# Performance work log

Measured on AMD Instinct MI355X. Metric: run time of the kernel, lower is better.

The kernel has to match this reference:

```python
import jax, jax.numpy as jnp
import numpy as np

B, N, F, H = 2, 2048, 1024, 16
HD = F // H
SQRT_D = float(np.sqrt(F))  # note: module scales by sqrt(in_c), not sqrt(head_dim)


def setup_inputs() -> dict:
    key = jax.random.key(0)
    ks = jax.random.split(key, 9)
    s = 1.0 / np.sqrt(F)
    mk = lambda k: jax.random.uniform(k, (F, F), jnp.float32, -s, s)
    mb = lambda k: jax.random.uniform(k, (F,), jnp.float32, -s, s)
    return {
        "x": jax.random.normal(ks[0], (B, N, F), jnp.float32),
        "Wq": mk(ks[1]), "bq": mb(ks[2]),
        "Wk": mk(ks[3]), "bk": mb(ks[4]),
        "Wv": mk(ks[5]), "bv": mb(ks[6]),
        "Wo": mk(ks[7]), "bo": mb(ks[8]),
    }


def reference(x, Wq, bq, Wk, bk, Wv, bv, Wo, bo):
    b, n, f = x.shape
    # projections (torch Linear: x @ W.T + b); view to (b, n, h, hd)
    q = (x @ Wq.T + bq).reshape(b, n, H, HD)
    k = (x @ Wk.T + bk).reshape(b, n, H, HD)
    v = (x @ Wv.T + bv).reshape(b, n, H, HD)
    score = jnp.einsum('bihd,bjhd->bhij', q, k)
    attn = jax.nn.softmax(score / SQRT_D, axis=-1)
    o = jnp.einsum('bhij,bjhd->bihd', attn, v).reshape(b, n, f)
    return o @ Wo.T + bo
```

## Files before the change

kernel.cpp:

```cpp
#include <hip/hip_runtime.h>
#include <hip/hip_bf16.h>
#include <stdint.h>
#include <stddef.h>

typedef __bf16 bf16;
typedef __attribute__((ext_vector_type(8))) __bf16 bf16x8;
typedef __attribute__((ext_vector_type(4))) __bf16 bf16x4;
typedef __attribute__((ext_vector_type(2))) __bf16 bf16x2;
typedef __attribute__((ext_vector_type(4))) float f32x4;

#define MFMA16(a, b, c) __builtin_amdgcn_mfma_f32_16x16x32_bf16(a, b, c, 0, 0, 0)

#define BB 2
#define SEQ 2048
#define FDIM 1024
#define NH 16
#define HD 64
#define M_TOK 4096
#define N_QKV 3072

#define CSC 0.04508422f

__device__ __forceinline__ void gll16(const bf16* g, bf16* l) {
    __builtin_amdgcn_global_load_lds(
        (const __attribute__((address_space(1))) void*)g,
        (__attribute__((address_space(3))) void*)l, 16, 0, 0);
}

__device__ __forceinline__ bf16 pack_bf16(float f) {
    uint32_t u = __builtin_bit_cast(uint32_t, f);
    uint16_t h = (uint16_t)((u + 0x8000u) >> 16);
    return __builtin_bit_cast(bf16, h);
}

__device__ __forceinline__ uint32_t pk2(float a, float b) {
#if __has_builtin(__builtin_amdgcn_cvt_pk_bf16_f32)
    bf16x2 t = __builtin_amdgcn_cvt_pk_bf16_f32(a, b);
    return __builtin_bit_cast(uint32_t, t);
#else
    uint32_t ua = __builtin_bit_cast(uint32_t, a) + 0x8000u;
    uint32_t ub = __builtin_bit_cast(uint32_t, b) + 0x8000u;
    return __builtin_amdgcn_perm(ub, ua, 0x07060302);
#endif
}

__global__ __launch_bounds__(256) void convert_k(
    const float* __restrict__ x,
    const float* __restrict__ Wq, const float* __restrict__ bq,
    const float* __restrict__ Wk, const float* __restrict__ bk,
    const float* __restrict__ Wv, const float* __restrict__ bv,
    const float* __restrict__ Wo,
    bf16* __restrict__ xb, bf16* __restrict__ Wcat, bf16* __restrict__ Wob,
    float* __restrict__ bcat)
{
    const int tid = blockIdx.x * blockDim.x + threadIdx.x;
    const int nt = gridDim.x * blockDim.x;
    const int NX4 = M_TOK * FDIM / 4;
    const int NW4 = FDIM * FDIM / 4;

    for (int i = tid; i < NX4; i += nt) {
        float4 v = ((const float4*)x)[i];
        bf16x4 o; o[0] = (bf16)v.x; o[1] = (bf16)v.y; o[2] = (bf16)v.z; o[3] = (bf16)v.w;
        ((bf16x4*)xb)[i] = o;
    }
    for (int i = tid; i < NW4; i += nt) {
        float4 v = ((const float4*)Wq)[i];
        bf16x4 o;
        o[0] = (bf16)(v.x * CSC); o[1] = (bf16)(v.y * CSC);
        o[2] = (bf16)(v.z * CSC); o[3] = (bf16)(v.w * CSC);
        ((bf16x4*)Wcat)[i] = o;
        v = ((const float4*)Wk)[i];
        o[0] = (bf16)v.x; o[1] = (bf16)v.y; o[2] = (bf16)v.z; o[3] = (bf16)v.w;
        ((bf16x4*)Wcat)[NW4 + i] = o;
        v = ((const float4*)Wv)[i];
        o[0] = (bf16)v.x; o[1] = (bf16)v.y; o[2] = (bf16)v.z; o[3] = (bf16)v.w;
        ((bf16x4*)Wcat)[2 * NW4 + i] = o;
        v = ((const float4*)Wo)[i];
        o[0] = (bf16)v.x; o[1] = (bf16)v.y; o[2] = (bf16)v.z; o[3] = (bf16)v.w;
        ((bf16x4*)Wob)[i] = o;
    }
    for (int i = tid; i < FDIM; i += nt) {
        bcat[i] = bq[i] * CSC;
        bcat[FDIM + i] = bk[i];
        bcat[2 * FDIM + i] = bv[i];
    }
}

__global__ __launch_bounds__(512, 2) void gemm256(
    const bf16* __restrict__ A,
    const bf16* __restrict__ Bw,
    const float* __restrict__ bias,
    bf16* __restrict__ Cb,
    bf16* __restrict__ VtOut,
    int M, int N, int K)
{
    extern __shared__ char smem[];
    const int tid = threadIdx.x;
    const int lane = tid & 63;
    const int wave = tid >> 6;
    const int wr = wave >> 2;
    const int wc = wave & 3;
    const int m0 = blockIdx.y * 256;
    const int n0 = blockIdx.x * 256;
    const int lrow = lane & 15;
    const int quad = lane >> 4;
    const int NT = K >> 6;

    const int l8 = lane >> 3;
    const int kx = ((lane & 7) ^ l8) << 3;
    const int lcl = wave * 16 + l8;

#define ASTG(sl, kt, mh, c) do { \
    const int _lc = lcl + (c) * 8; \
    const int _gr = m0 + ((_lc >> 6) << 7) + ((mh) << 6) + (_lc & 63); \
    gll16(A + (size_t)_gr * K + (size_t)(kt) * 64 + kx, \
          (bf16*)(smem + (sl) * 65536 + (mh) * 16384 + wave * 2048 + (c) * 1024)); \
} while (0)
#define BSTG(sl, kt, nh, c) do { \
    const int _lc = lcl + (c) * 8; \
    const int _gc = n0 + ((_lc >> 5) << 6) + ((nh) << 5) + (_lc & 31); \
    gll16(Bw + (size_t)_gc * K + (size_t)(kt) * 64 + kx, \
          (bf16*)(smem + (sl) * 65536 + 32768 + (nh) * 16384 + wave * 2048 + (c) * 1024)); \
} while (0)

    const int swz0 = ((quad ^ (lrow & 7)) << 4);
    const int swz1 = (((4 + quad) ^ (lrow & 7)) << 4);
    const int arow = (wr * 64 + lrow) * 128;
    const int brow = (wc * 32 + lrow) * 128;

    f32x4 acc[8][4] = {};
    bf16x8 af[4][2];
    bf16x8 bc[2][2][2];

    ASTG(0, 0, 0, 0); ASTG(0, 0, 0, 1);
    BSTG(0, 0, 0, 0); BSTG(0, 0, 0, 1);
    BSTG(0, 0, 1, 0); BSTG(0, 0, 1, 1);
    ASTG(0, 0, 1, 0); ASTG(0, 0, 1, 1);
    asm volatile("s_waitcnt vmcnt(4)" ::: "memory");
    __builtin_amdgcn_s_barrier();

    for (int t = 0; t < NT; ++t) {
        const int sl = t & 1;
        const int ns = sl ^ 1;
        const char* sb = smem + sl * 65536;
        const bool pf = (t + 1 < NT);

#pragma unroll
        for (int ph = 0; ph < 4; ++ph) {
            const int mh = ph >> 1, nh = ph & 1;
            if (pf) {
                if (ph == 0)      { ASTG(ns, t + 1, 0, 0); ASTG(ns, t + 1, 0, 1); }
                else if (ph == 1) { BSTG(ns, t + 1, 0, 0); BSTG(ns, t + 1, 0, 1); }
                else if (ph == 2) { BSTG(ns, t + 1, 1, 0); BSTG(ns, t + 1, 1, 1); }
                else              { ASTG(ns, t + 1, 1, 0); ASTG(ns, t + 1, 1, 1); }
            }
            if (nh == 0) {
#pragma unroll
                for (int iq = 0; iq < 4; ++iq) {
                    af[iq][0] = *(const bf16x8*)(sb + mh * 16384 + arow + iq * 2048 + swz0);
                    af[iq][1] = *(const bf16x8*)(sb + mh * 16384 + arow + iq * 2048 + swz1);
                }
            }
            if (ph == 0 || ph == 1) {
#pragma unroll
                for (int jq = 0; jq < 2; ++jq) {
                    bc[nh][jq][0] = *(const bf16x8*)(sb + 32768 + nh * 16384 + brow + jq * 2048 + swz0);
                    bc[nh][jq][1] = *(const bf16x8*)(sb + 32768 + nh * 16384 + brow + jq * 2048 + swz1);
                }
            }
            __builtin_amdgcn_s_setprio(1);
#pragma unroll
            for (int iq = 0; iq < 4; ++iq)
#pragma unroll
                for (int jq = 0; jq < 2; ++jq) {
                    acc[mh * 4 + iq][nh * 2 + jq] =
                        MFMA16(af[iq][0], bc[nh][jq][0], acc[mh * 4 + iq][nh * 2 + jq]);
                    acc[mh * 4 + iq][nh * 2 + jq] =
                        MFMA16(af[iq][1], bc[nh][jq][1], acc[mh * 4 + iq][nh * 2 + jq]);
                }
            __builtin_amdgcn_s_setprio(0);
            if (pf) asm volatile("s_waitcnt vmcnt(4)" ::: "memory");
            else    asm volatile("s_waitcnt vmcnt(0)" ::: "memory");
            __builtin_amdgcn_s_barrier();
        }
    }
#undef ASTG
#undef BSTG

    if (VtOut && n0 >= 2048) {
        const int bql = (m0 >> 11);
#pragma unroll
        for (int i = 0; i < 8; ++i) {
#pragma unroll
            for (int j = 0; j < 4; ++j) {
                const int col = n0 + wc * 64 + (j >> 1) * 32 + (j & 1) * 16 + lrow;
                const float bsv = bias[col];
                const int vh = col - 2048;
                const int row = m0 + wr * 128 + (i >> 2) * 64 + (i & 3) * 16 + quad * 4;
                const int jj = row & (SEQ - 1);
                const int g = jj & 63;
                const int jj2 = (jj & ~63) | ((g >> 5) << 5)
                              | (((g >> 2) & 3) << 3) | (((g >> 4) & 1) << 2);
                bf16x4 vv;
#pragma unroll
                for (int r = 0; r < 4; ++r)
                    vv[r] = pack_bf16(acc[i][j][r] + bsv);
                *(bf16x4*)&VtOut[((size_t)bql * 16 * 64 + vh) * SEQ + jj2] = vv;
            }
        }
        return;
    }
#pragma unroll
    for (int i = 0; i < 8; ++i) {
#pragma unroll
        for (int j = 0; j < 4; ++j) {
            const int col = n0 + wc * 64 + (j >> 1) * 32 + (j & 1) * 16 + lrow;
            const float bsv = bias[col];
#pragma unroll
            for (int r = 0; r < 4; ++r) {
                const int row = m0 + wr * 128 + (i >> 2) * 64 + (i & 3) * 16 + quad * 4 + r;
                Cb[(size_t)row * N + col] = pack_bf16(acc[i][j][r] + bsv);
            }
        }
    }
}

template<int MT>
__global__ __launch_bounds__(256) void gemm_bt(
    const bf16* __restrict__ A,
    const bf16* __restrict__ Bw,
    const float* __restrict__ bias,
    float* __restrict__ Cf,
    int M, int N, int K)
{
    constexpr int RI = MT / 32;
    __shared__ __align__(16) bf16 As[2][MT * 32];
    __shared__ __align__(16) bf16 Bs[2][128 * 32];

    const int tid = threadIdx.x;
    const int lane = tid & 63;
    const int wave = tid >> 6;
    const int m0 = blockIdx.y * MT;
    const int n0 = blockIdx.x * 128;
    const int wm = (wave >> 1) * (MT / 2);
    const int wn = (wave & 1) * 64;
    const int lrow = lane & 15;
    const int quad = lane >> 4;

    f32x4 acc[RI][4] = {};

    const int srow = wave * 16 + (lane >> 2);
    const int scol = ((lane & 3) ^ ((lane >> 3) & 3)) * 8;
    const bf16* Ag = A + (size_t)(m0 + srow) * K + scol;
    const bf16* Bg = Bw + (size_t)(n0 + srow) * K + scol;
    const int wo = (wave * 16) * 32;
    const int swz8 = (quad ^ ((lrow >> 1) & 3)) * 8;

    gll16(Ag, &As[0][wo]);
    if (MT == 128) gll16(Ag + (size_t)64 * K, &As[0][wo + 2048]);
    gll16(Bg, &Bs[0][wo]);
    gll16(Bg + (size_t)64 * K, &Bs[0][wo + 2048]);

    for (int k0 = 0, it = 0; k0 < K; k0 += 32, ++it) {
        const int cur = it & 1;
        __syncthreads();

        if (k0 + 32 < K) {
            const int nxt = cur ^ 1;
            gll16(Ag + k0 + 32, &As[nxt][wo]);
            if (MT == 128) gll16(Ag + (size_t)64 * K + k0 + 32, &As[nxt][wo + 2048]);
            gll16(Bg + k0 + 32, &Bs[nxt][wo]);
            gll16(Bg + (size_t)64 * K + k0 + 32, &Bs[nxt][wo + 2048]);
        }

        bf16x8 af[RI], bfr[4];
#pragma unroll
        for (int s = 0; s < RI; ++s)
            af[s] = *(const bf16x8*)&As[cur][(wm + s * 16 + lrow) * 32 + swz8];
#pragma unroll
        for (int s = 0; s < 4; ++s)
            bfr[s] = *(const bf16x8*)&Bs[cur][(wn + s * 16 + lrow) * 32 + swz8];
#pragma unroll
        for (int i = 0; i < RI; ++i)
#pragma unroll
            for (int j = 0; j < 4; ++j)
                acc[i][j] = MFMA16(af[i], bfr[j], acc[i][j]);
    }

    const int r0 = quad * 4;
#pragma unroll
    for (int i = 0; i < RI; ++i) {
#pragma unroll
        for (int j = 0; j < 4; ++j) {
            const int col = n0 + wn + j * 16 + lrow;
            const float bsv = bias[col];
#pragma unroll
            for (int r = 0; r < 4; ++r) {
                const int row = m0 + wm + i * 16 + r0 + r;
                Cf[(size_t)row * N + col] = acc[i][j][r] + bsv;
            }
        }
    }
}

__global__ __launch_bounds__(512, 4) void attn_k(
    const bf16* __restrict__ QKV,
    const bf16* __restrict__ Vt,
    bf16* __restrict__ O)
{
    const int bx = blockIdx.x;
    const int bh = (bx & 7) + 8 * ((bx >> 3) & 3);
    const int qblk = bx >> 5;
    const int b = bh >> 4;
    const int h = bh & 15;
    const int lane = threadIdx.x & 63;
    const int wave = threadIdx.x >> 6;
    const int qg = wave & 3;
    const int jp = wave >> 2;
    const int lrow = lane & 15;
    const int quad = lane >> 4;
    const int lk8 = quad * 8;

    __shared__ __align__(16) bf16 Ks[2][2][128 * 32];
    __shared__ __align__(16) bf16 Vs[2][4][64 * 32];

    const size_t base = (size_t)b * SEQ * N_QKV;
    const bf16* Qp = QKV + base + h * HD;
    const bf16* Kp = QKV + base + FDIM + h * HD;
    const bf16* Vtp = Vt + (size_t)bh * HD * SEQ;

    const int qr0 = qblk * 128 + qg * 32;

    bf16x8 qf[2][2];
#pragma unroll
    for (int qt = 0; qt < 2; ++qt)
#pragma unroll
        for (int ks = 0; ks < 2; ++ks)
            qf[qt][ks] = *(const bf16x8*)(Qp + (size_t)(qr0 + qt * 16 + lrow) * N_QKV
                                          + ks * 32 + lk8);

    bf16x8 ones8;
#pragma unroll
    for (int e = 0; e < 8; ++e) ones8[e] = (bf16)1.0f;

    const f32x4 zf = {0.f, 0.f, 0.f, 0.f};

    f32x4 o[2][4] = {};
    f32x4 o4[2] = {};

    const int srow = wave * 16 + (lane >> 2);
    const int scol = ((lane & 3) ^ ((lane >> 3) & 3)) * 8;
    const bf16* kg = Kp + (size_t)srow * N_QKV + scol;
    const int vsrow = qg * 16 + (lane >> 2);
    const bf16* vg = Vtp + (size_t)vsrow * SEQ + jp * 32 + scol;
    const int kwo = wave * 512;
    const int swz8 = (quad ^ ((lrow >> 1) & 3)) * 8;

    gll16(kg,      &Ks[0][0][0] + kwo);
    gll16(kg + 32, &Ks[0][1][0] + kwo);
    gll16(vg,      &Vs[0][0][0] + kwo);
    gll16(vg + 64, &Vs[0][2][0] + kwo);
    kg += (size_t)128 * N_QKV;
    vg += 128;

    for (int jt = 0; jt < SEQ / 128; ++jt) {
        const int cur = jt & 1;
        __syncthreads();

        if (jt + 1 < SEQ / 128) {
            const int nxt = cur ^ 1;
            gll16(kg,      &Ks[nxt][0][0] + kwo);
            gll16(kg + 32, &Ks[nxt][1][0] + kwo);
            gll16(vg,      &Vs[nxt][0][0] + kwo);
            gll16(vg + 64, &Vs[nxt][2][0] + kwo);
            kg += (size_t)128 * N_QKV;
            vg += 128;
        }

#pragma unroll
        for (int pp = 0; pp < 2; ++pp) {
            const int p = (pp << 1) | jp;
            f32x4 Sp[2][2];
            __builtin_amdgcn_s_setprio(1);
#pragma unroll
            for (int m = 0; m < 2; ++m) {
                const int jn = 2 * p + m;
                bf16x8 kb0 = *(const bf16x8*)&Ks[cur][0][(jn * 16 + lrow) * 32 + swz8];
                bf16x8 kb1 = *(const bf16x8*)&Ks[cur][1][(jn * 16 + lrow) * 32 + swz8];
                Sp[m][0] = MFMA16(kb0, qf[0][0], zf);
                Sp[m][0] = MFMA16(kb1, qf[0][1], Sp[m][0]);
                Sp[m][1] = MFMA16(kb0, qf[1][0], zf);
                Sp[m][1] = MFMA16(kb1, qf[1][1], Sp[m][1]);
            }
            __builtin_amdgcn_s_setprio(0);

            union { bf16x8 v; uint32_t d[4]; } pb[2];
#pragma unroll
            for (int qt = 0; qt < 2; ++qt) {
                const f32x4 s0 = Sp[0][qt];
                const f32x4 s1 = Sp[1][qt];
                pb[qt].d[0] = pk2(__builtin_amdgcn_exp2f(s0[0]),
                                  __builtin_amdgcn_exp2f(s0[1]));
                pb[qt].d[1] = pk2(__builtin_amdgcn_exp2f(s0[2]),
                                  __builtin_amdgcn_exp2f(s0[3]));
                pb[qt].d[2] = pk2(__builtin_amdgcn_exp2f(s1[0]),
                                  __builtin_amdgcn_exp2f(s1[1]));
                pb[qt].d[3] = pk2(__builtin_amdgcn_exp2f(s1[2]),
                                  __builtin_amdgcn_exp2f(s1[3]));
            }

            __builtin_amdgcn_s_setprio(1);
            o4[0] = MFMA16(ones8, pb[0].v, o4[0]);
            o4[1] = MFMA16(ones8, pb[1].v, o4[1]);
#pragma unroll
            for (int df = 0; df < 4; ++df) {
                bf16x8 vA = *(const bf16x8*)&Vs[cur][p][(df * 16 + lrow) * 32 + swz8];
                o[0][df] = MFMA16(vA, pb[0].v, o[0][df]);
                o[1][df] = MFMA16(vA, pb[1].v, o[1][df]);
            }
            __builtin_amdgcn_s_setprio(0);
        }
    }

    __syncthreads();
    float* shO = (float*)Ks;
    float* shS = (float*)Vs;
    if (jp == 1) {
#pragma unroll
        for (int qt = 0; qt < 2; ++qt)
#pragma unroll
            for (int df = 0; df < 4; ++df)
                *(f32x4*)&shO[((((qt * 4 + df) * 4) + qg) * 64 + lane) * 4] = o[qt][df];
        shS[(qg * 64 + lane) * 2 + 0] = o4[0][0];
        shS[(qg * 64 + lane) * 2 + 1] = o4[1][0];
    }
    __syncthreads();
    if (jp == 1) return;

#pragma unroll
    for (int qt = 0; qt < 2; ++qt)
#pragma unroll
        for (int df = 0; df < 4; ++df) {
            f32x4 t = *(const f32x4*)&shO[((((qt * 4 + df) * 4) + qg) * 64 + lane) * 4];
            o[qt][df][0] += t[0]; o[qt][df][1] += t[1];
            o[qt][df][2] += t[2]; o[qt][df][3] += t[3];
        }
    const float den0 = o4[0][0] + shS[(qg * 64 + lane) * 2 + 0];
    const float den1 = o4[1][0] + shS[(qg * 64 + lane) * 2 + 1];

#pragma unroll
    for (int qt = 0; qt < 2; ++qt) {
        const float inv = 1.0f / (qt ? den1 : den0);
        const int q = qr0 + qt * 16 + lrow;
#pragma unroll
        for (int df = 0; df < 4; ++df) {
            bf16x4 vv;
#pragma unroll
            for (int r = 0; r < 4; ++r)
                vv[r] = pack_bf16(o[qt][df][r] * inv);
            *(bf16x4*)&O[(size_t)(b * SEQ + q) * FDIM + h * HD + df * 16 + quad * 4] = vv;
        }
    }
}

extern "C" void kernel_launch(void* const* d_in, const int* in_sizes, int n_in,
                              void* d_out, int out_size, void* d_ws, size_t ws_size,
                              hipStream_t stream) {
    (void)in_sizes; (void)n_in; (void)out_size; (void)ws_size;
    const float* x  = (const float*)d_in[0];
    const float* Wq = (const float*)d_in[1];
    const float* bq = (const float*)d_in[2];
    const float* Wk = (const float*)d_in[3];
    const float* bk = (const float*)d_in[4];
    const float* Wv = (const float*)d_in[5];
    const float* bv = (const float*)d_in[6];
    const float* Wo = (const float*)d_in[7];
    const float* bo = (const float*)d_in[8];
    float* out = (float*)d_out;

    char* ws = (char*)d_ws;
    bf16* xb    = (bf16*)(ws);
    bf16* Wcat  = (bf16*)(ws + 8388608);
    bf16* Wob   = (bf16*)(ws + 14680064);
    float* bcat = (float*)(ws + 16777216);
    bf16* QKV   = (bf16*)(ws + 16789504);
    bf16* Vt    = (bf16*)(ws + 41955328);
    bf16* Ob    = xb;

    static bool s_attr_done = false;
    if (!s_attr_done) {
        (void)hipFuncSetAttribute(reinterpret_cast<const void*>(gemm256),
                                  hipFuncAttributeMaxDynamicSharedMemorySize,
                                  131072);
        s_attr_done = true;
    }

    convert_k<<<dim3(1024), dim3(256), 0, stream>>>(x, Wq, bq, Wk, bk, Wv, bv, Wo,
                                                    xb, Wcat, Wob, bcat);
    gemm256<<<dim3(N_QKV / 256, M_TOK / 256), dim3(512), 131072, stream>>>(
        xb, Wcat, bcat, QKV, Vt, M_TOK, N_QKV, FDIM);
    attn_k<<<dim3((SEQ / 128) * BB * NH), dim3(512), 0, stream>>>(QKV, Vt, Ob);
    gemm_bt<64><<<dim3(FDIM / 128, M_TOK / 64), dim3(256), 0, stream>>>(
        Ob, Wob, bo, out, M_TOK, FDIM, FDIM);
}
```

Measured before the change: 184.5 us.

## Split attention key tiles across four wave groups with 1024-thread blocks

Doubles the attention block to 16 waves so each of four wave groups handles one 32-key slice of each 128-key tile, instead of two groups each looping over two slices. K/V staging loads are redistributed so each wave issues one global-to-LDS load per tile, and the final partial-sum merge becomes a serialized three-step reduction through shared memory. This aims to add parallelism and latency hiding per block, but launch_bounds(1024,8) may force register spills, and the extra syncs in the reduction add overhead.

```diff
diff --git a/kernel.cpp b/kernel.cpp
--- a/kernel.cpp
+++ b/kernel.cpp
@@ -303,7 +303,7 @@
     }
 }
 
-__global__ __launch_bounds__(512, 4) void attn_k(
+__global__ __launch_bounds__(1024, 8) void attn_k(
     const bf16* __restrict__ QKV,
     const bf16* __restrict__ Vt,
     bf16* __restrict__ O)
@@ -348,18 +348,19 @@
     f32x4 o[2][4] = {};
     f32x4 o4[2] = {};
 
-    const int srow = wave * 16 + (lane >> 2);
+    const int sl4 = lane >> 2;
     const int scol = ((lane & 3) ^ ((lane >> 3) & 3)) * 8;
-    const bf16* kg = Kp + (size_t)srow * N_QKV + scol;
-    const int vsrow = qg * 16 + (lane >> 2);
+    const int ksrow = (wave & 7) * 16 + sl4;
+    const bf16* kg = Kp + (size_t)ksrow * N_QKV + (wave >> 3) * 32 + scol;
+    char* const kd0 = (char*)&Ks[0][0][0] + (wave >> 3) * 8192 + (wave & 7) * 1024;
+    const int vsrow = (wave & 3) * 16 + sl4;
     const bf16* vg = Vtp + (size_t)vsrow * SEQ + jp * 32 + scol;
-    const int kwo = wave * 512;
+    char* const vd0 = (char*)&Vs[0][0][0] + jp * 4096 + (wave & 3) * 1024;
+
     const int swz8 = (quad ^ ((lrow >> 1) & 3)) * 8;
 
-    gll16(kg,      &Ks[0][0][0] + kwo);
-    gll16(kg + 32, &Ks[0][1][0] + kwo);
-    gll16(vg,      &Vs[0][0][0] + kwo);
-    gll16(vg + 64, &Vs[0][2][0] + kwo);
+    gll16(kg, (bf16*)kd0);
+    gll16(vg, (bf16*)vd0);
     kg += (size_t)128 * N_QKV;
     vg += 128;
 
@@ -369,73 +370,82 @@
 
         if (jt + 1 < SEQ / 128) {
             const int nxt = cur ^ 1;
-            gll16(kg,      &Ks[nxt][0][0] + kwo);
-            gll16(kg + 32, &Ks[nxt][1][0] + kwo);
-            gll16(vg,      &Vs[nxt][0][0] + kwo);
-            gll16(vg + 64, &Vs[nxt][2][0] + kwo);
+            gll16(kg, (bf16*)(kd0 + nxt * 16384));
+            gll16(vg, (bf16*)(vd0 + nxt * 16384));
             kg += (size_t)128 * N_QKV;
             vg += 128;
         }
 
-#pragma unroll
-        for (int pp = 0; pp < 2; ++pp) {
-            const int p = (pp << 1) | jp;
-            f32x4 Sp[2][2];
-            __builtin_amdgcn_s_setprio(1);
-#pragma unroll
-            for (int m = 0; m < 2; ++m) {
-                const int jn = 2 * p + m;
-                bf16x8 kb0 = *(const bf16x8*)&Ks[cur][0][(jn * 16 + lrow) * 32 + swz8];
-                bf16x8 kb1 = *(const bf16x8*)&Ks[cur][1][(jn * 16 + lrow) * 32 + swz8];
-                Sp[m][0] = MFMA16(kb0, qf[0][0], zf);
-                Sp[m][0] = MFMA16(kb1, qf[0][1], Sp[m][0]);
-                Sp[m][1] = MFMA16(kb0, qf[1][0], zf);
-                Sp[m][1] = MFMA16(kb1, qf[1][1], Sp[m][1]);
-            }
-            __builtin_amdgcn_s_setprio(0);
-
-            union { bf16x8 v; uint32_t d[4]; } pb[2];
-#pragma unroll
-            for (int qt = 0; qt < 2; ++qt) {
-                const f32x4 s0 = Sp[0][qt];
-                const f32x4 s1 = Sp[1][qt];
-                pb[qt].d[0] = pk2(__builtin_amdgcn_exp2f(s0[0]),
-                                  __builtin_amdgcn_exp2f(s0[1]));
-                pb[qt].d[1] = pk2(__builtin_amdgcn_exp2f(s0[2]),
-                                  __builtin_amdgcn_exp2f(s0[3]));
-                pb[qt].d[2] = pk2(__builtin_amdgcn_exp2f(s1[0]),
-                                  __builtin_amdgcn_exp2f(s1[1]));
-                pb[qt].d[3] = pk2(__builtin_amdgcn_exp2f(s1[2]),
-                                  __builtin_amdgcn_exp2f(s1[3]));
-            }
-
-            __builtin_amdgcn_s_setprio(1);
-            o4[0] = MFMA16(ones8, pb[0].v, o4[0]);
-            o4[1] = MFMA16(ones8, pb[1].v, o4[1]);
-#pragma unroll
-            for (int df = 0; df < 4; ++df) {
-                bf16x8 vA = *(const bf16x8*)&Vs[cur][p][(df * 16 + lrow) * 32 + swz8];
-                o[0][df] = MFMA16(vA, pb[0].v, o[0][df]);
-                o[1][df] = MFMA16(vA, pb[1].v, o[1][df]);
-            }
-            __builtin_amdgcn_s_setprio(0);
-        }
+        f32x4 Sp[2][2];
+        __builtin_amdgcn_s_setprio(1);
+#pragma unroll
+        for (int m = 0; m < 2; ++m) {
+            const int jn = 2 * jp + m;
+            bf16x8 kb0 = *(const bf16x8*)&Ks[cur][0][(jn * 16 + lrow) * 32 + swz8];
+            bf16x8 kb1 = *(const bf16x8*)&Ks[cur][1][(jn * 16 + lrow) * 32 + swz8];
+            Sp[m][0] = MFMA16(kb0, qf[0][0], zf);
+            Sp[m][0] = MFMA16(kb1, qf[0][1], Sp[m][0]);
+            Sp[m][1] = MFMA16(kb0, qf[1][0], zf);
+            Sp[m][1] = MFMA16(kb1, qf[1][1], Sp[m][1]);
+        }
+        __builtin_amdgcn_s_setprio(0);
+
+        union { bf16x8 v; uint32_t d[4]; } pb[2];
+#pragma unroll
+        for (int qt = 0; qt < 2; ++qt) {
+            const f32x4 s0 = Sp[0][qt];
+            const f32x4 s1 = Sp[1][qt];
+            pb[qt].d[0] = pk2(__builtin_amdgcn_exp2f(s0[0]),
+                              __builtin_amdgcn_exp2f(s0[1]));
+            pb[qt].d[1] = pk2(__builtin_amdgcn_exp2f(s0[2]),
+                              __builtin_amdgcn_exp2f(s0[3]));
+            pb[qt].d[2] = pk2(__builtin_amdgcn_exp2f(s1[0]),
+                              __builtin_amdgcn_exp2f(s1[1]));
+            pb[qt].d[3] = pk2(__builtin_amdgcn_exp2f(s1[2]),
+                              __builtin_amdgcn_exp2f(s1[3]));
+        }
+
+        __builtin_amdgcn_s_setprio(1);
+        o4[0] = MFMA16(ones8, pb[0].v, o4[0]);
+        o4[1] = MFMA16(ones8, pb[1].v, o4[1]);
+#pragma unroll
+        for (int df = 0; df < 4; ++df) {
+            bf16x8 vA = *(const bf16x8*)&Vs[cur][jp][(df * 16 + lrow) * 32 + swz8];
+            o[0][df] = MFMA16(vA, pb[0].v, o[0][df]);
+            o[1][df] = MFMA16(vA, pb[1].v, o[1][df]);
+        }
+        __builtin_amdgcn_s_setprio(0);
     }
 
     __syncthreads();
     float* shO = (float*)Ks;
     float* shS = (float*)Vs;
-    if (jp == 1) {
-#pragma unroll
-        for (int qt = 0; qt < 2; ++qt)
-#pragma unroll
-            for (int df = 0; df < 4; ++df)
-                *(f32x4*)&shO[((((qt * 4 + df) * 4) + qg) * 64 + lane) * 4] = o[qt][df];
-        shS[(qg * 64 + lane) * 2 + 0] = o4[0][0];
-        shS[(qg * 64 + lane) * 2 + 1] = o4[1][0];
-    }
-    __syncthreads();
-    if (jp == 1) return;
+#pragma unroll
+    for (int r = 3; r >= 1; --r) {
+        if (jp == r) {
+            if (r < 3) {
+#pragma unroll
+                for (int qt = 0; qt < 2; ++qt)
+#pragma unroll
+                    for (int df = 0; df < 4; ++df) {
+                        f32x4 t = *(const f32x4*)&shO[((((qt * 4 + df) * 4) + qg) * 64 + lane) * 4];
+                        o[qt][df][0] += t[0]; o[qt][df][1] += t[1];
+                        o[qt][df][2] += t[2]; o[qt][df][3] += t[3];
+                    }
+                o4[0][0] += shS[(qg * 64 + lane) * 2 + 0];
+                o4[1][0] += shS[(qg * 64 + lane) * 2 + 1];
+            }
+#pragma unroll
+            for (int qt = 0; qt < 2; ++qt)
+#pragma unroll
+                for (int df = 0; df < 4; ++df)
+                    *(f32x4*)&shO[((((qt * 4 + df) * 4) + qg) * 64 + lane) * 4] = o[qt][df];
+            shS[(qg * 64 + lane) * 2 + 0] = o4[0][0];
+            shS[(qg * 64 + lane) * 2 + 1] = o4[1][0];
+        }
+        __syncthreads();
+    }
+    if (jp != 0) return;
 
 #pragma unroll
     for (int qt = 0; qt < 2; ++qt)
@@ -499,7 +509,7 @@
                                                     xb, Wcat, Wob, bcat);
     gemm256<<<dim3(N_QKV / 256, M_TOK / 256), dim3(512), 131072, stream>>>(
         xb, Wcat, bcat, QKV, Vt, M_TOK, N_QKV, FDIM);
-    attn_k<<<dim3((SEQ / 128) * BB * NH), dim3(512), 0, stream>>>(QKV, Vt, Ob);
+    attn_k<<<dim3((SEQ / 128) * BB * NH), dim3(1024), 0, stream>>>(QKV, Vt, Ob);
     gemm_bt<64><<<dim3(FDIM / 128, M_TOK / 64), dim3(256), 0, stream>>>(
         Ob, Wob, bo, out, M_TOK, FDIM, FDIM);
 }
```

Result: slower. 454.5 us (+146.4%).
